# Kernel optimization log

Measured on AMD Instinct MI355X. Metric: run time of the kernel, lower is better.

Reference implementation:

```python
import jax, jax.numpy as jnp
import numpy as np

B, NVIS, NHID, NCLASS = 2048, 2048, 1024, 64


def setup_inputs() -> dict:
    key = jax.random.key(0)
    k1, k2, k3, k4, k5 = jax.random.split(key, 5)
    return {
        "v": jax.random.normal(k1, (B, NVIS), dtype=jnp.float32),
        "W": jax.random.normal(k2, (NVIS, NHID), dtype=jnp.float32),
        "c": jax.random.normal(k3, (1, NHID), dtype=jnp.float32),
        "d": jax.random.normal(k4, (1, NCLASS), dtype=jnp.float32),
        "U": jax.random.normal(k5, (NCLASS, NHID), dtype=jnp.float32),
    }


def reference(v, W, c, d, U):
    # precomputed_factor: [B, nhid]
    pre = jnp.matmul(v, W) + c
    # class free energies F[b, y] = d[0, y] + sum_j softplus(pre[b, j] + U[y, j])
    # broadcast to [B, nclass, nhid], reduce over hidden units
    F = d[0] + jnp.sum(jax.nn.softplus(pre[:, None, :] + U[None, :, :]), axis=-1)  # [B, nclass]
    # pairwise normalization 1 / sum_d exp(F_d - F_c) == softmax(F) along classes
    class_probs = jax.nn.softmax(F, axis=1)
    max_idx = jnp.argmax(class_probs, axis=1)
    one_hot = jax.nn.one_hot(max_idx, U.shape[0], dtype=jnp.int32)
    return class_probs, one_hot
```

## Files before the change

### kernel.cpp

```cpp
#include <hip/hip_runtime.h>

constexpr int kB    = 2048;
constexpr int kVIS  = 2048;
constexpr int kHID  = 1024;
constexpr int kCLS  = 64;
constexpr float kLog2e = 1.4426950408889634f;

typedef __attribute__((ext_vector_type(8))) short bf16x8;
typedef __attribute__((ext_vector_type(4))) float f32x4;
typedef __attribute__((ext_vector_type(2))) float f32x2;

typedef __attribute__((address_space(3))) unsigned       as3_u32;
typedef __attribute__((address_space(1))) const unsigned as1_u32;

__device__ __forceinline__ void g2lds16(const void* g, void* l) {
    __builtin_amdgcn_global_load_lds((as1_u32*)g, (as3_u32*)l, 16, 0, 0);
}

__device__ __forceinline__ unsigned short f2bf(float x) {
    unsigned u = __float_as_uint(x);
    u += 0x7fffu + ((u >> 16) & 1u);
    return (unsigned short)(u >> 16);
}
__device__ __forceinline__ float bf2f(unsigned short h) {
    return __uint_as_float(((unsigned)h) << 16);
}

__global__ __launch_bounds__(256) void prep_all(const float* __restrict__ v,
                                                const float* __restrict__ W,
                                                const float* __restrict__ U,
                                                unsigned short* __restrict__ vh,
                                                unsigned short* __restrict__ vl,
                                                unsigned short* __restrict__ wth,
                                                unsigned short* __restrict__ wtl,
                                                float* __restrict__ Utp) {
    __shared__ float T[64][65];
    const int bx = blockIdx.x;
    if (bx < 4096) {
        const int i = (bx * 256 + threadIdx.x) * 4;
        const float4 xv = *(const float4*)(v + i);
        ushort4 h, l;
        h.x = f2bf(xv.x); l.x = f2bf(xv.x - bf2f(h.x));
        h.y = f2bf(xv.y); l.y = f2bf(xv.y - bf2f(h.y));
        h.z = f2bf(xv.z); l.z = f2bf(xv.z - bf2f(h.z));
        h.w = f2bf(xv.w); l.w = f2bf(xv.w - bf2f(h.w));
        *(ushort4*)(vh + i) = h;
        *(ushort4*)(vl + i) = l;
    } else if (bx < 4608) {
        const int b = bx - 4096;
        const int n0 = (b & 15) * 64;
        const int k0 = (b >> 4) * 64;
        const int c = threadIdx.x & 63, r0 = threadIdx.x >> 6;
#pragma unroll
        for (int ps = 0; ps < 16; ++ps) {
            const int r = r0 + ps * 4;
            T[r][c] = W[(size_t)(k0 + r) * kHID + n0 + c];
        }
        __syncthreads();
#pragma unroll
        for (int ps = 0; ps < 16; ++ps) {
            const int nn = r0 + ps * 4;
            const float x = T[c][nn];
            const unsigned short h = f2bf(x);
            const unsigned short l = f2bf(x - bf2f(h));
            const size_t o = (size_t)(n0 + nn) * kVIS + k0 + c;
            wth[o] = h;
            wtl[o] = l;
        }
    } else {
        const int id = (bx - 4608) * 256 + threadIdx.x;
        const int j = id >> 6, y = id & 63;
        Utp[(((j >> 2) * kCLS + y) << 2) + (j & 3)] = U[(size_t)y * kHID + j] * kLog2e;
    }
}

__global__ __launch_bounds__(512, 4) void gemm_fused(const unsigned short* __restrict__ vh,
                                                     const unsigned short* __restrict__ vl,
                                                     const unsigned short* __restrict__ wth,
                                                     const unsigned short* __restrict__ wtl,
                                                     const float* __restrict__ cvec,
                                                     const float* __restrict__ Utp,
                                                     float* __restrict__ Fpart) {
    __shared__ __align__(16) union SMem {
        unsigned short stage[2][4][64 * 64];
        float psH[2][64][68];
    } smem;

    const int tid = threadIdx.x;
    const int lane = tid & 63, wave = tid >> 6;
    const int mh = wave >> 2;
    const int nh = (wave >> 1) & 1;
    const int kh = wave & 1;

    const int bid = blockIdx.x;
    const int idx = bid >> 3;
    const int mstripe = ((bid & 7) << 2) + (idx >> 4);
    const int ncol = idx & 15;
    const int m0 = mstripe * 64, n0 = ncol * 64;

    const int r = tid >> 3;
    const int oc = (((tid & 7) ^ ((tid >> 3) & 7)) << 3);
    const size_t ga = (size_t)(m0 + r) * kVIS + oc;
    const size_t gb = (size_t)(n0 + r) * kVIS + oc;
    const int ls = (r << 6) + ((tid & 7) << 3);

    const int fm = lane & 15, fq = lane >> 4;
    const int rx = fm & 7;
    const int ar0 = (mh * 32 + fm) << 6, ar1 = (mh * 32 + 16 + fm) << 6;
    const int br0 = (nh * 32 + fm) << 6, br1 = (nh * 32 + 16 + fm) << 6;
    const int p = (((kh << 2) + fq) ^ rx) << 3;

    f32x4 acc[2][2] = {};

    {
        g2lds16(vh + ga,  smem.stage[0][0] + ls);
        g2lds16(vl + ga,  smem.stage[0][1] + ls);
        g2lds16(wth + gb, smem.stage[0][2] + ls);
        g2lds16(wtl + gb, smem.stage[0][3] + ls);
    }
    __syncthreads();

    int cur = 0;
    for (int k0 = 0; k0 < kVIS; k0 += 64) {
        if (k0 + 64 < kVIS) {
            const int ko = k0 + 64;
            g2lds16(vh + ga + ko,  smem.stage[cur ^ 1][0] + ls);
            g2lds16(vl + ga + ko,  smem.stage[cur ^ 1][1] + ls);
            g2lds16(wth + gb + ko, smem.stage[cur ^ 1][2] + ls);
            g2lds16(wtl + gb + ko, smem.stage[cur ^ 1][3] + ls);
        }
        const unsigned short* Ah = smem.stage[cur][0];
        const unsigned short* Al = smem.stage[cur][1];
        const unsigned short* Bh = smem.stage[cur][2];
        const unsigned short* Bl = smem.stage[cur][3];
        const bf16x8 a_h0 = *(const bf16x8*)(Ah + ar0 + p);
        const bf16x8 a_h1 = *(const bf16x8*)(Ah + ar1 + p);
        const bf16x8 a_l0 = *(const bf16x8*)(Al + ar0 + p);
        const bf16x8 a_l1 = *(const bf16x8*)(Al + ar1 + p);
        const bf16x8 b_h0 = *(const bf16x8*)(Bh + br0 + p);
        const bf16x8 b_h1 = *(const bf16x8*)(Bh + br1 + p);
        const bf16x8 b_l0 = *(const bf16x8*)(Bl + br0 + p);
        const bf16x8 b_l1 = *(const bf16x8*)(Bl + br1 + p);
        acc[0][0] = __builtin_amdgcn_mfma_f32_16x16x32_bf16(a_h0, b_h0, acc[0][0], 0, 0, 0);
        acc[0][0] = __builtin_amdgcn_mfma_f32_16x16x32_bf16(a_h0, b_l0, acc[0][0], 0, 0, 0);
        acc[0][0] = __builtin_amdgcn_mfma_f32_16x16x32_bf16(a_l0, b_h0, acc[0][0], 0, 0, 0);
        acc[0][1] = __builtin_amdgcn_mfma_f32_16x16x32_bf16(a_h0, b_h1, acc[0][1], 0, 0, 0);
        acc[0][1] = __builtin_amdgcn_mfma_f32_16x16x32_bf16(a_h0, b_l1, acc[0][1], 0, 0, 0);
        acc[0][1] = __builtin_amdgcn_mfma_f32_16x16x32_bf16(a_l0, b_h1, acc[0][1], 0, 0, 0);
        acc[1][0] = __builtin_amdgcn_mfma_f32_16x16x32_bf16(a_h1, b_h0, acc[1][0], 0, 0, 0);
        acc[1][0] = __builtin_amdgcn_mfma_f32_16x16x32_bf16(a_h1, b_l0, acc[1][0], 0, 0, 0);
        acc[1][0] = __builtin_amdgcn_mfma_f32_16x16x32_bf16(a_l1, b_h0, acc[1][0], 0, 0, 0);
        acc[1][1] = __builtin_amdgcn_mfma_f32_16x16x32_bf16(a_h1, b_h1, acc[1][1], 0, 0, 0);
        acc[1][1] = __builtin_amdgcn_mfma_f32_16x16x32_bf16(a_h1, b_l1, acc[1][1], 0, 0, 0);
        acc[1][1] = __builtin_amdgcn_mfma_f32_16x16x32_bf16(a_l1, b_h1, acc[1][1], 0, 0, 0);
        __syncthreads();
        cur ^= 1;
    }

#pragma unroll
    for (int j = 0; j < 2; ++j) {
        const int col = nh * 32 + j * 16 + fm;
        const float cadd = kh ? 0.f : cvec[n0 + col];
#pragma unroll
        for (int i = 0; i < 2; ++i) {
            const int rbase = mh * 32 + i * 16 + fq * 4;
#pragma unroll
            for (int rr = 0; rr < 4; ++rr)
                smem.psH[kh][rbase + rr][col] = (acc[i][j][rr] + cadd) * kLog2e;
        }
    }
    __syncthreads();

#pragma unroll
    for (int s = 0; s < 2; ++s) {
        const int id = tid + (s << 9);
        const int row = id >> 4, q = id & 15;
        float4* d = (float4*)&smem.psH[0][row][q << 2];
        const float4* a = (const float4*)&smem.psH[1][row][q << 2];
        const float4 va = *a, vd = *d;
        *d = make_float4(vd.x + va.x, vd.y + va.y, vd.z + va.z, vd.w + va.w);
    }
    __syncthreads();

    const int q0 = (n0 >> 2);
    f32x2 relu2[8], prod2[8];
#pragma unroll
    for (int rr = 0; rr < 8; ++rr) { relu2[rr] = (f32x2)(0.f); prod2[rr] = (f32x2)(1.f); }

    const f32x2 zero2 = (f32x2)(0.f);
    for (int jc = 0; jc < 64; jc += 8) {
        const float4 ua = ((const float4*)Utp)[(q0 + (jc >> 2) + 0) * kCLS + lane];
        const float4 ub = ((const float4*)Utp)[(q0 + (jc >> 2) + 1) * kCLS + lane];
        const f32x2 u01 = {ua.x, ua.y}, u23 = {ua.z, ua.w};
        const f32x2 u45 = {ub.x, ub.y}, u67 = {ub.z, ub.w};
#pragma unroll
        for (int rr = 0; rr < 8; ++rr) {
            const int row = wave * 8 + rr;
            const float4 p0 = *(const float4*)&smem.psH[0][row][jc];
            const float4 p1 = *(const float4*)&smem.psH[0][row][jc + 4];
            f32x2 tp[4];
            tp[0] = (f32x2){p0.x, p0.y} + u01;
            tp[1] = (f32x2){p0.z, p0.w} + u23;
            tp[2] = (f32x2){p1.x, p1.y} + u45;
            tp[3] = (f32x2){p1.z, p1.w} + u67;
#pragma unroll
            for (int g = 0; g < 4; ++g) {
                const f32x2 t = tp[g];
                f32x2 e;
                e.x = __builtin_amdgcn_exp2f(-__builtin_fabsf(t.x));
                e.y = __builtin_amdgcn_exp2f(-__builtin_fabsf(t.y));
                prod2[rr] = __builtin_elementwise_fma(prod2[rr], e, prod2[rr]);
                relu2[rr] += __builtin_elementwise_max(t, zero2);
            }
        }
    }
#pragma unroll
    for (int rr = 0; rr < 8; ++rr) {
        const float contrib = relu2[rr].x + relu2[rr].y +
                              __builtin_amdgcn_logf(prod2[rr].x * prod2[rr].y);
        Fpart[((size_t)ncol * kB + m0 + wave * 8 + rr) * kCLS + lane] = contrib;
    }
}

__global__ __launch_bounds__(256) void softmax_final(const float* __restrict__ Fpart,
                                                     const float* __restrict__ dvec,
                                                     float* __restrict__ out) {
    const int tid = threadIdx.x;
    const int lane = tid & 63, wave = tid >> 6;
    const int row = blockIdx.x * 4 + wave;
    double s = 0.0;
#pragma unroll
    for (int k = 0; k < kHID / 64; ++k)
        s += (double)Fpart[((size_t)k * kB + row) * kCLS + lane];
    const float G = (float)s + dvec[lane] * kLog2e;

    float m = G;
    int mi = lane;
#pragma unroll
    for (int off = 32; off; off >>= 1) {
        const float om = __shfl_xor(m, off);
        const int   oi = __shfl_xor(mi, off);
        if (om > m || (om == m && oi < mi)) { m = om; mi = oi; }
    }
    const float e2 = __builtin_amdgcn_exp2f(G - m);
    float ssum = e2;
#pragma unroll
    for (int off = 32; off; off >>= 1) ssum += __shfl_xor(ssum, off);
    out[(size_t)row * kCLS + lane] = e2 / ssum;
    out[(size_t)kB * kCLS + (size_t)row * kCLS + lane] = (lane == mi) ? 1.0f : 0.0f;
}

constexpr int BM = 64, BN = 64, BK = 16;

__global__ __launch_bounds__(256) void gemm_vw(const float* __restrict__ V,
                                               const float* __restrict__ Wm,
                                               const float* __restrict__ cvec,
                                               float* __restrict__ pre) {
    __shared__ float As[BK][BM + 4];
    __shared__ float Bs[BK][BN + 4];
    const int tid = threadIdx.x;
    const int tx = tid & 15, ty = tid >> 4;
    const int m0 = blockIdx.y * BM, n0 = blockIdx.x * BN;
    const int arow = tid >> 2, acol = (tid & 3) << 2;
    const int brow = tid >> 4, bcol = (tid & 15) << 2;
    const float* vptr = V + (size_t)(m0 + arow) * kVIS + acol;
    const float* wptr = Wm + (size_t)brow * kHID + n0 + bcol;
    float acc[4][4] = {};
    for (int k0 = 0; k0 < kVIS; k0 += BK) {
        const float4 a4 = *(const float4*)(vptr + k0);
        const float4 b4 = *(const float4*)(wptr + (size_t)k0 * kHID);
        __syncthreads();
        As[acol + 0][arow] = a4.x; As[acol + 1][arow] = a4.y;
        As[acol + 2][arow] = a4.z; As[acol + 3][arow] = a4.w;
        *(float4*)&Bs[brow][bcol] = b4;
        __syncthreads();
#pragma unroll
        for (int k = 0; k < BK; ++k) {
            const float4 av = *(const float4*)&As[k][ty << 2];
            const float4 bv = *(const float4*)&Bs[k][tx << 2];
            const float a[4] = {av.x, av.y, av.z, av.w};
            const float b[4] = {bv.x, bv.y, bv.z, bv.w};
#pragma unroll
            for (int i = 0; i < 4; ++i)
#pragma unroll
                for (int j = 0; j < 4; ++j) acc[i][j] += a[i] * b[j];
        }
    }
#pragma unroll
    for (int i = 0; i < 4; ++i) {
        const int row = m0 + (ty << 2) + i;
        const int col = n0 + (tx << 2);
        const float4 cv = *(const float4*)(cvec + col);
        float4 o;
        o.x = acc[i][0] + cv.x; o.y = acc[i][1] + cv.y;
        o.z = acc[i][2] + cv.z; o.w = acc[i][3] + cv.w;
        *(float4*)(pre + (size_t)row * kHID + col) = o;
    }
}

__device__ __forceinline__ float softplus_f(float x) {
    return fmaxf(x, 0.f) + __logf(1.f + __expf(-fabsf(x)));
}

__global__ __launch_bounds__(256) void classify(const float* __restrict__ pre,
                                                const float* __restrict__ U,
                                                const float* __restrict__ dvec,
                                                float* __restrict__ out) {
    __shared__ float preS[4][kHID];
    __shared__ float Fs[4][kCLS];
    const int tid = threadIdx.x;
    const int lane = tid & 63, wave = tid >> 6;
    const int b0 = blockIdx.x * 4;
    const float4* src = (const float4*)(pre + (size_t)b0 * kHID);
    float4* dst = (float4*)preS;
    for (int i = tid; i < kHID; i += 256) dst[i] = src[i];
    __syncthreads();
    for (int yi = 0; yi < 16; ++yi) {
        const int y = (wave << 4) + yi;
        const float* Uy = U + (size_t)y * kHID;
        float a0 = 0.f, a1 = 0.f, a2 = 0.f, a3 = 0.f;
#pragma unroll
        for (int it = 0; it < kHID / 64; ++it) {
            const int j = lane + (it << 6);
            const float u = Uy[j];
            a0 += softplus_f(preS[0][j] + u);
            a1 += softplus_f(preS[1][j] + u);
            a2 += softplus_f(preS[2][j] + u);
            a3 += softplus_f(preS[3][j] + u);
        }
        double d0 = a0, d1 = a1, d2 = a2, d3 = a3;
#pragma unroll
        for (int off = 32; off; off >>= 1) {
            d0 += __shfl_xor(d0, off); d1 += __shfl_xor(d1, off);
            d2 += __shfl_xor(d2, off); d3 += __shfl_xor(d3, off);
        }
        if (lane == 0) {
            const float dy = dvec[y];
            Fs[0][y] = (float)d0 + dy; Fs[1][y] = (float)d1 + dy;
            Fs[2][y] = (float)d2 + dy; Fs[3][y] = (float)d3 + dy;
        }
    }
    __syncthreads();
    const float F = Fs[wave][lane];
    float m = F; int mi = lane;
#pragma unroll
    for (int off = 32; off; off >>= 1) {
        const float om = __shfl_xor(m, off);
        const int oi = __shfl_xor(mi, off);
        if (om > m || (om == m && oi < mi)) { m = om; mi = oi; }
    }
    const float e = __expf(F - m);
    float s = e;
#pragma unroll
    for (int off = 32; off; off >>= 1) s += __shfl_xor(s, off);
    const int row = b0 + wave;
    out[(size_t)row * kCLS + lane] = e / s;
    out[(size_t)kB * kCLS + (size_t)row * kCLS + lane] = (lane == mi) ? 1.0f : 0.0f;
}

extern "C" void kernel_launch(void* const* d_in, const int* in_sizes, int n_in,
                              void* d_out, int out_size, void* d_ws, size_t ws_size,
                              hipStream_t stream) {
    const float* v = (const float*)d_in[0];
    const float* W = (const float*)d_in[1];
    const float* c = (const float*)d_in[2];
    const float* d = (const float*)d_in[3];
    const float* U = (const float*)d_in[4];
    float* out = (float*)d_out;
    char* ws = (char*)d_ws;

    const size_t need = 33816576;
    if (ws_size >= need) {
        unsigned short* vh  = (unsigned short*)(ws);
        unsigned short* vl  = (unsigned short*)(ws + 8388608);
        unsigned short* wth = (unsigned short*)(ws + 16777216);
        unsigned short* wtl = (unsigned short*)(ws + 20971520);
        float* Utp   = (float*)(ws + 25165824);
        float* Fpart = (float*)(ws + 25427968);
        prep_all<<<4864, 256, 0, stream>>>(v, W, U, vh, vl, wth, wtl, Utp);
        gemm_fused<<<512, 512, 0, stream>>>(vh, vl, wth, wtl, c, Utp, Fpart);
        softmax_final<<<kB / 4, 256, 0, stream>>>(Fpart, d, out);
    } else {
        float* pre = (float*)ws;
        gemm_vw<<<dim3(kHID / BN, kB / BM), 256, 0, stream>>>(v, W, c, pre);
        classify<<<kB / 4, 256, 0, stream>>>(pre, U, d, out);
    }
}
```

Before: 130.0 us.

## Fuse prep, GEMM and softmax into one cooperative kernel with grid syncs

Merges the three kernel launches (bf16 split/transpose prep, fused GEMM+softplus, softmax/argmax) into a single cooperative kernel of 512 blocks. The stages are separated by grid-wide barriers, which removes launch gaps and inter-kernel drain. The old three-kernel path stays as a fallback if the cooperative launch fails. The cost is two grid syncs and all blocks having to be co-resident. The prep stage now runs with a fixed 512-block shape, and the softmax stage uses only half the waves of each block.

```diff
diff --git a/kernel.cpp b/kernel.cpp
--- a/kernel.cpp
+++ b/kernel.cpp
@@ -1,4 +1,7 @@
 #include <hip/hip_runtime.h>
+#include <hip/hip_cooperative_groups.h>
+
+namespace cg = cooperative_groups;
 
 constexpr int kB    = 2048;
 constexpr int kVIS  = 2048;
@@ -26,73 +29,76 @@
     return __uint_as_float(((unsigned)h) << 16);
 }
 
-__global__ __launch_bounds__(256) void prep_all(const float* __restrict__ v,
-                                                const float* __restrict__ W,
-                                                const float* __restrict__ U,
-                                                unsigned short* __restrict__ vh,
-                                                unsigned short* __restrict__ vl,
-                                                unsigned short* __restrict__ wth,
-                                                unsigned short* __restrict__ wtl,
-                                                float* __restrict__ Utp) {
-    __shared__ float T[64][65];
-    const int bx = blockIdx.x;
-    if (bx < 4096) {
-        const int i = (bx * 256 + threadIdx.x) * 4;
-        const float4 xv = *(const float4*)(v + i);
-        ushort4 h, l;
-        h.x = f2bf(xv.x); l.x = f2bf(xv.x - bf2f(h.x));
-        h.y = f2bf(xv.y); l.y = f2bf(xv.y - bf2f(h.y));
-        h.z = f2bf(xv.z); l.z = f2bf(xv.z - bf2f(h.z));
-        h.w = f2bf(xv.w); l.w = f2bf(xv.w - bf2f(h.w));
-        *(ushort4*)(vh + i) = h;
-        *(ushort4*)(vl + i) = l;
-    } else if (bx < 4608) {
-        const int b = bx - 4096;
-        const int n0 = (b & 15) * 64;
-        const int k0 = (b >> 4) * 64;
-        const int c = threadIdx.x & 63, r0 = threadIdx.x >> 6;
-#pragma unroll
-        for (int ps = 0; ps < 16; ++ps) {
-            const int r = r0 + ps * 4;
-            T[r][c] = W[(size_t)(k0 + r) * kHID + n0 + c];
+__global__ __launch_bounds__(512, 4) void fused_all(const float* __restrict__ v,
+                                                    const float* __restrict__ W,
+                                                    const float* __restrict__ U,
+                                                    const float* __restrict__ cvec,
+                                                    const float* __restrict__ dvec,
+                                                    unsigned short* __restrict__ vh,
+                                                    unsigned short* __restrict__ vl,
+                                                    unsigned short* __restrict__ wth,
+                                                    unsigned short* __restrict__ wtl,
+                                                    float* __restrict__ Utp,
+                                                    float* __restrict__ Fpart,
+                                                    float* __restrict__ out) {
+    __shared__ __align__(16) union SMem {
+        unsigned short stage[2][4][64 * 64];
+        float psH[2][64][68];
+        float T[64][65];
+    } smem;
+
+    const int tid = threadIdx.x;
+    const int bid = blockIdx.x;
+    const int lane = tid & 63, wave = tid >> 6;
+
+    {
+        const int gthr = bid * 512 + tid;
+#pragma unroll
+        for (int it = 0; it < 4; ++it) {
+            const int i = (gthr + it * 262144) * 4;
+            const float4 xv = *(const float4*)(v + i);
+            ushort4 h, l;
+            h.x = f2bf(xv.x); l.x = f2bf(xv.x - bf2f(h.x));
+            h.y = f2bf(xv.y); l.y = f2bf(xv.y - bf2f(h.y));
+            h.z = f2bf(xv.z); l.z = f2bf(xv.z - bf2f(h.z));
+            h.w = f2bf(xv.w); l.w = f2bf(xv.w - bf2f(h.w));
+            *(ushort4*)(vh + i) = h;
+            *(ushort4*)(vl + i) = l;
+        }
+    }
+    {
+        const int n0 = (bid & 15) * 64;
+        const int k0 = (bid >> 4) * 64;
+        const int c = lane, r0 = wave;
+#pragma unroll
+        for (int ps = 0; ps < 8; ++ps) {
+            const int r = r0 + ps * 8;
+            smem.T[r][c] = W[(size_t)(k0 + r) * kHID + n0 + c];
         }
         __syncthreads();
 #pragma unroll
-        for (int ps = 0; ps < 16; ++ps) {
-            const int nn = r0 + ps * 4;
-            const float x = T[c][nn];
+        for (int ps = 0; ps < 8; ++ps) {
+            const int nn = r0 + ps * 8;
+            const float x = smem.T[c][nn];
             const unsigned short h = f2bf(x);
             const unsigned short l = f2bf(x - bf2f(h));
             const size_t o = (size_t)(n0 + nn) * kVIS + k0 + c;
             wth[o] = h;
             wtl[o] = l;
         }
-    } else {
-        const int id = (bx - 4608) * 256 + threadIdx.x;
+    }
+    if (tid < 128) {
+        const int id = bid * 128 + tid;
         const int j = id >> 6, y = id & 63;
         Utp[(((j >> 2) * kCLS + y) << 2) + (j & 3)] = U[(size_t)y * kHID + j] * kLog2e;
     }
-}
-
-__global__ __launch_bounds__(512, 4) void gemm_fused(const unsigned short* __restrict__ vh,
-                                                     const unsigned short* __restrict__ vl,
-                                                     const unsigned short* __restrict__ wth,
-                                                     const unsigned short* __restrict__ wtl,
-                                                     const float* __restrict__ cvec,
-                                                     const float* __restrict__ Utp,
-                                                     float* __restrict__ Fpart) {
-    __shared__ __align__(16) union SMem {
-        unsigned short stage[2][4][64 * 64];
-        float psH[2][64][68];
-    } smem;
-
-    const int tid = threadIdx.x;
-    const int lane = tid & 63, wave = tid >> 6;
+
+    cg::this_grid().sync();
+
     const int mh = wave >> 2;
     const int nh = (wave >> 1) & 1;
     const int kh = wave & 1;
 
-    const int bid = blockIdx.x;
     const int idx = bid >> 3;
     const int mstripe = ((bid & 7) << 2) + (idx >> 4);
     const int ncol = idx & 15;
@@ -220,6 +226,228 @@
                               __builtin_amdgcn_logf(prod2[rr].x * prod2[rr].y);
         Fpart[((size_t)ncol * kB + m0 + wave * 8 + rr) * kCLS + lane] = contrib;
     }
+
+    cg::this_grid().sync();
+
+    if (wave < 4) {
+        const int row = bid * 4 + wave;
+        double s = 0.0;
+#pragma unroll
+        for (int k = 0; k < kHID / 64; ++k)
+            s += (double)Fpart[((size_t)k * kB + row) * kCLS + lane];
+        const float G = (float)s + dvec[lane] * kLog2e;
+
+        float m = G;
+        int mi = lane;
+#pragma unroll
+        for (int off = 32; off; off >>= 1) {
+            const float om = __shfl_xor(m, off);
+            const int   oi = __shfl_xor(mi, off);
+            if (om > m || (om == m && oi < mi)) { m = om; mi = oi; }
+        }
+        const float e2 = __builtin_amdgcn_exp2f(G - m);
+        float ssum = e2;
+#pragma unroll
+        for (int off = 32; off; off >>= 1) ssum += __shfl_xor(ssum, off);
+        out[(size_t)row * kCLS + lane] = e2 / ssum;
+        out[(size_t)kB * kCLS + (size_t)row * kCLS + lane] = (lane == mi) ? 1.0f : 0.0f;
+    }
+}
+
+__global__ __launch_bounds__(256) void prep_all(const float* __restrict__ v,
+                                                const float* __restrict__ W,
+                                                const float* __restrict__ U,
+                                                unsigned short* __restrict__ vh,
+                                                unsigned short* __restrict__ vl,
+                                                unsigned short* __restrict__ wth,
+                                                unsigned short* __restrict__ wtl,
+                                                float* __restrict__ Utp) {
+    __shared__ float T[64][65];
+    const int bx = blockIdx.x;
+    if (bx < 4096) {
+        const int i = (bx * 256 + threadIdx.x) * 4;
+        const float4 xv = *(const float4*)(v + i);
+        ushort4 h, l;
+        h.x = f2bf(xv.x); l.x = f2bf(xv.x - bf2f(h.x));
+        h.y = f2bf(xv.y); l.y = f2bf(xv.y - bf2f(h.y));
+        h.z = f2bf(xv.z); l.z = f2bf(xv.z - bf2f(h.z));
+        h.w = f2bf(xv.w); l.w = f2bf(xv.w - bf2f(h.w));
+        *(ushort4*)(vh + i) = h;
+        *(ushort4*)(vl + i) = l;
+    } else if (bx < 4608) {
+        const int b = bx - 4096;
+        const int n0 = (b & 15) * 64;
+        const int k0 = (b >> 4) * 64;
+        const int c = threadIdx.x & 63, r0 = threadIdx.x >> 6;
+#pragma unroll
+        for (int ps = 0; ps < 16; ++ps) {
+            const int r = r0 + ps * 4;
+            T[r][c] = W[(size_t)(k0 + r) * kHID + n0 + c];
+        }
+        __syncthreads();
+#pragma unroll
+        for (int ps = 0; ps < 16; ++ps) {
+            const int nn = r0 + ps * 4;
+            const float x = T[c][nn];
+            const unsigned short h = f2bf(x);
+            const unsigned short l = f2bf(x - bf2f(h));
+            const size_t o = (size_t)(n0 + nn) * kVIS + k0 + c;
+            wth[o] = h;
+            wtl[o] = l;
+        }
+    } else {
+        const int id = (bx - 4608) * 256 + threadIdx.x;
+        const int j = id >> 6, y = id & 63;
+        Utp[(((j >> 2) * kCLS + y) << 2) + (j & 3)] = U[(size_t)y * kHID + j] * kLog2e;
+    }
+}
+
+__global__ __launch_bounds__(512, 4) void gemm_fused(const unsigned short* __restrict__ vh,
+                                                     const unsigned short* __restrict__ vl,
+                                                     const unsigned short* __restrict__ wth,
+                                                     const unsigned short* __restrict__ wtl,
+                                                     const float* __restrict__ cvec,
+                                                     const float* __restrict__ Utp,
+                                                     float* __restrict__ Fpart) {
+    __shared__ __align__(16) union SMem {
+        unsigned short stage[2][4][64 * 64];
+        float psH[2][64][68];
+    } smem;
+
+    const int tid = threadIdx.x;
+    const int lane = tid & 63, wave = tid >> 6;
+    const int mh = wave >> 2;
+    const int nh = (wave >> 1) & 1;
+    const int kh = wave & 1;
+
+    const int bid = blockIdx.x;
+    const int idx = bid >> 3;
+    const int mstripe = ((bid & 7) << 2) + (idx >> 4);
+    const int ncol = idx & 15;
+    const int m0 = mstripe * 64, n0 = ncol * 64;
+
+    const int r = tid >> 3;
+    const int oc = (((tid & 7) ^ ((tid >> 3) & 7)) << 3);
+    const size_t ga = (size_t)(m0 + r) * kVIS + oc;
+    const size_t gb = (size_t)(n0 + r) * kVIS + oc;
+    const int ls = (r << 6) + ((tid & 7) << 3);
+
+    const int fm = lane & 15, fq = lane >> 4;
+    const int rx = fm & 7;
+    const int ar0 = (mh * 32 + fm) << 6, ar1 = (mh * 32 + 16 + fm) << 6;
+    const int br0 = (nh * 32 + fm) << 6, br1 = (nh * 32 + 16 + fm) << 6;
+    const int p = (((kh << 2) + fq) ^ rx) << 3;
+
+    f32x4 acc[2][2] = {};
+
+    {
+        g2lds16(vh + ga,  smem.stage[0][0] + ls);
+        g2lds16(vl + ga,  smem.stage[0][1] + ls);
+        g2lds16(wth + gb, smem.stage[0][2] + ls);
+        g2lds16(wtl + gb, smem.stage[0][3] + ls);
+    }
+    __syncthreads();
+
+    int cur = 0;
+    for (int k0 = 0; k0 < kVIS; k0 += 64) {
+        if (k0 + 64 < kVIS) {
+            const int ko = k0 + 64;
+            g2lds16(vh + ga + ko,  smem.stage[cur ^ 1][0] + ls);
+            g2lds16(vl + ga + ko,  smem.stage[cur ^ 1][1] + ls);
+            g2lds16(wth + gb + ko, smem.stage[cur ^ 1][2] + ls);
+            g2lds16(wtl + gb + ko, smem.stage[cur ^ 1][3] + ls);
+        }
+        const unsigned short* Ah = smem.stage[cur][0];
+        const unsigned short* Al = smem.stage[cur][1];
+        const unsigned short* Bh = smem.stage[cur][2];
+        const unsigned short* Bl = smem.stage[cur][3];
+        const bf16x8 a_h0 = *(const bf16x8*)(Ah + ar0 + p);
+        const bf16x8 a_h1 = *(const bf16x8*)(Ah + ar1 + p);
+        const bf16x8 a_l0 = *(const bf16x8*)(Al + ar0 + p);
+        const bf16x8 a_l1 = *(const bf16x8*)(Al + ar1 + p);
+        const bf16x8 b_h0 = *(const bf16x8*)(Bh + br0 + p);
+        const bf16x8 b_h1 = *(const bf16x8*)(Bh + br1 + p);
+        const bf16x8 b_l0 = *(const bf16x8*)(Bl + br0 + p);
+        const bf16x8 b_l1 = *(const bf16x8*)(Bl + br1 + p);
+        acc[0][0] = __builtin_amdgcn_mfma_f32_16x16x32_bf16(a_h0, b_h0, acc[0][0], 0, 0, 0);
+        acc[0][0] = __builtin_amdgcn_mfma_f32_16x16x32_bf16(a_h0, b_l0, acc[0][0], 0, 0, 0);
+        acc[0][0] = __builtin_amdgcn_mfma_f32_16x16x32_bf16(a_l0, b_h0, acc[0][0], 0, 0, 0);
+        acc[0][1] = __builtin_amdgcn_mfma_f32_16x16x32_bf16(a_h0, b_h1, acc[0][1], 0, 0, 0);
+        acc[0][1] = __builtin_amdgcn_mfma_f32_16x16x32_bf16(a_h0, b_l1, acc[0][1], 0, 0, 0);
+        acc[0][1] = __builtin_amdgcn_mfma_f32_16x16x32_bf16(a_l0, b_h1, acc[0][1], 0, 0, 0);
+        acc[1][0] = __builtin_amdgcn_mfma_f32_16x16x32_bf16(a_h1, b_h0, acc[1][0], 0, 0, 0);
+        acc[1][0] = __builtin_amdgcn_mfma_f32_16x16x32_bf16(a_h1, b_l0, acc[1][0], 0, 0, 0);
+        acc[1][0] = __builtin_amdgcn_mfma_f32_16x16x32_bf16(a_l1, b_h0, acc[1][0], 0, 0, 0);
+        acc[1][1] = __builtin_amdgcn_mfma_f32_16x16x32_bf16(a_h1, b_h1, acc[1][1], 0, 0, 0);
+        acc[1][1] = __builtin_amdgcn_mfma_f32_16x16x32_bf16(a_h1, b_l1, acc[1][1], 0, 0, 0);
+        acc[1][1] = __builtin_amdgcn_mfma_f32_16x16x32_bf16(a_l1, b_h1, acc[1][1], 0, 0, 0);
+        __syncthreads();
+        cur ^= 1;
+    }
+
+#pragma unroll
+    for (int j = 0; j < 2; ++j) {
+        const int col = nh * 32 + j * 16 + fm;
+        const float cadd = kh ? 0.f : cvec[n0 + col];
+#pragma unroll
+        for (int i = 0; i < 2; ++i) {
+            const int rbase = mh * 32 + i * 16 + fq * 4;
+#pragma unroll
+            for (int rr = 0; rr < 4; ++rr)
+                smem.psH[kh][rbase + rr][col] = (acc[i][j][rr] + cadd) * kLog2e;
+        }
+    }
+    __syncthreads();
+
+#pragma unroll
+    for (int s = 0; s < 2; ++s) {
+        const int id = tid + (s << 9);
+        const int row = id >> 4, q = id & 15;
+        float4* d = (float4*)&smem.psH[0][row][q << 2];
+        const float4* a = (const float4*)&smem.psH[1][row][q << 2];
+        const float4 va = *a, vd = *d;
+        *d = make_float4(vd.x + va.x, vd.y + va.y, vd.z + va.z, vd.w + va.w);
+    }
+    __syncthreads();
+
+    const int q0 = (n0 >> 2);
+    f32x2 relu2[8], prod2[8];
+#pragma unroll
+    for (int rr = 0; rr < 8; ++rr) { relu2[rr] = (f32x2)(0.f); prod2[rr] = (f32x2)(1.f); }
+
+    const f32x2 zero2 = (f32x2)(0.f);
+    for (int jc = 0; jc < 64; jc += 8) {
+        const float4 ua = ((const float4*)Utp)[(q0 + (jc >> 2) + 0) * kCLS + lane];
+        const float4 ub = ((const float4*)Utp)[(q0 + (jc >> 2) + 1) * kCLS + lane];
+        const f32x2 u01 = {ua.x, ua.y}, u23 = {ua.z, ua.w};
+        const f32x2 u45 = {ub.x, ub.y}, u67 = {ub.z, ub.w};
+#pragma unroll
+        for (int rr = 0; rr < 8; ++rr) {
+            const int row = wave * 8 + rr;
+            const float4 p0 = *(const float4*)&smem.psH[0][row][jc];
+            const float4 p1 = *(const float4*)&smem.psH[0][row][jc + 4];
+            f32x2 tp[4];
+            tp[0] = (f32x2){p0.x, p0.y} + u01;
+            tp[1] = (f32x2){p0.z, p0.w} + u23;
+            tp[2] = (f32x2){p1.x, p1.y} + u45;
+            tp[3] = (f32x2){p1.z, p1.w} + u67;
+#pragma unroll
+            for (int g = 0; g < 4; ++g) {
+                const f32x2 t = tp[g];
+                f32x2 e;
+                e.x = __builtin_amdgcn_exp2f(-__builtin_fabsf(t.x));
+                e.y = __builtin_amdgcn_exp2f(-__builtin_fabsf(t.y));
+                prod2[rr] = __builtin_elementwise_fma(prod2[rr], e, prod2[rr]);
+                relu2[rr] += __builtin_elementwise_max(t, zero2);
+            }
+        }
+    }
+#pragma unroll
+    for (int rr = 0; rr < 8; ++rr) {
+        const float contrib = relu2[rr].x + relu2[rr].y +
+                              __builtin_amdgcn_logf(prod2[rr].x * prod2[rr].y);
+        Fpart[((size_t)ncol * kB + m0 + wave * 8 + rr) * kCLS + lane] = contrib;
+    }
 }
 
 __global__ __launch_bounds__(256) void softmax_final(const float* __restrict__ Fpart,
@@ -377,9 +605,18 @@
         unsigned short* wtl = (unsigned short*)(ws + 20971520);
         float* Utp   = (float*)(ws + 25165824);
         float* Fpart = (float*)(ws + 25427968);
-        prep_all<<<4864, 256, 0, stream>>>(v, W, U, vh, vl, wth, wtl, Utp);
-        gemm_fused<<<512, 512, 0, stream>>>(vh, vl, wth, wtl, c, Utp, Fpart);
-        softmax_final<<<kB / 4, 256, 0, stream>>>(Fpart, d, out);
+
+        void* kargs[] = {(void*)&v, (void*)&W, (void*)&U, (void*)&c, (void*)&d,
+                         (void*)&vh, (void*)&vl, (void*)&wth, (void*)&wtl,
+                         (void*)&Utp, (void*)&Fpart, (void*)&out};
+        hipError_t err = hipLaunchCooperativeKernel((const void*)fused_all,
+                                                    dim3(512), dim3(512),
+                                                    kargs, 0, stream);
+        if (err != hipSuccess) {
+            prep_all<<<4864, 256, 0, stream>>>(v, W, U, vh, vl, wth, wtl, Utp);
+            gemm_fused<<<512, 512, 0, stream>>>(vh, vl, wth, wtl, c, Utp, Fpart);
+            softmax_final<<<kB / 4, 256, 0, stream>>>(Fpart, d, out);
+        }
     } else {
         float* pre = (float*)ws;
         gemm_vw<<<dim3(kHID / BN, kB / BM), 256, 0, stream>>>(v, W, c, pre);
```

Measured after the change: 252.2 us. 1.94x slower.

## Use four-stage LDS ring with k-step-32 tiles and parity-split waves

Applied to the files above, without the earlier changes.

The GEMM mainloop now streams K in 32-wide chunks that pack hi and lo bf16 halves into one 64-column tile. Chunks go into a 4-deep LDS ring and are prefetched two steps ahead, with explicit vmcnt waits and a raw s_barrier in place of a full __syncthreads per step. Instead of splitting each K tile across wave pairs, even and odd waves alternate consuming whole chunks. This keeps more loads in flight and cuts barrier cost, but only half the waves issue MFMAs on any given step.

```diff
diff --git a/kernel.cpp b/kernel.cpp
--- a/kernel.cpp
+++ b/kernel.cpp
@@ -82,7 +82,7 @@
                                                      const float* __restrict__ Utp,
                                                      float* __restrict__ Fpart) {
     __shared__ __align__(16) union SMem {
-        unsigned short stage[2][4][64 * 64];
+        unsigned short stage[4][8192];
         float psH[2][64][68];
     } smem;
 
@@ -90,7 +90,7 @@
     const int lane = tid & 63, wave = tid >> 6;
     const int mh = wave >> 2;
     const int nh = (wave >> 1) & 1;
-    const int kh = wave & 1;
+    const int pw = wave & 1;
 
     const int bid = blockIdx.x;
     const int idx = bid >> 3;
@@ -98,49 +98,78 @@
     const int ncol = idx & 15;
     const int m0 = mstripe * 64, n0 = ncol * 64;
 
-    const int r = tid >> 3;
-    const int oc = (((tid & 7) ^ ((tid >> 3) & 7)) << 3);
-    const size_t ga = (size_t)(m0 + r) * kVIS + oc;
-    const size_t gb = (size_t)(n0 + r) * kVIS + oc;
-    const int ls = (r << 6) + ((tid & 7) << 3);
+    unsigned short* const st = &smem.stage[0][0];
+
+    {
+    }
+    const int sr = tid >> 3;
+    const int sq = tid & 7;
+    const int su = sq ^ (sr & 7);
+    const int soct = su & 3;
+    const unsigned short* srcA =
+        ((su >> 2) ? vl : vh) + (size_t)(m0 + sr) * kVIS + (soct << 3);
+    const unsigned short* srcB =
+        ((su >> 2) ? wtl : wth) + (size_t)(n0 + sr) * kVIS + (soct << 3);
+    const int lsA = tid << 3;
+    const int lsB = 4096 + (tid << 3);
 
     const int fm = lane & 15, fq = lane >> 4;
-    const int rx = fm & 7;
-    const int ar0 = (mh * 32 + fm) << 6, ar1 = (mh * 32 + 16 + fm) << 6;
-    const int br0 = (nh * 32 + fm) << 6, br1 = (nh * 32 + 16 + fm) << 6;
-    const int p = (((kh << 2) + fq) ^ rx) << 3;
+    const int ph = ((fq ^ (fm & 7)) << 3);
+    const int pl = ph ^ 32;
+    const int ar0 = (mh * 32 + fm) << 6, ar1 = ar0 + 1024;
+    const int br0 = 4096 + ((nh * 32 + fm) << 6), br1 = br0 + 1024;
 
     f32x4 acc[2][2] = {};
 
+    g2lds16(srcA, st + lsA);
+    g2lds16(srcB, st + lsB);
+    g2lds16(srcA + 32, st + 8192 + lsA);
+    g2lds16(srcB + 32, st + 8192 + lsB);
+
+    for (int t = 0; t < 62; ++t) {
+        const int koff = (t + 2) << 5;
+        unsigned short* const dst = st + (((t + 2) & 3) << 13);
+        g2lds16(srcA + koff, dst + lsA);
+        g2lds16(srcB + koff, dst + lsB);
+        asm volatile("s_waitcnt vmcnt(4)" ::: "memory");
+        __builtin_amdgcn_s_barrier();
+        if (pw == (t & 1)) {
+            const unsigned short* buf = st + ((t & 3) << 13);
+            const bf16x8 a_h0 = *(const bf16x8*)(buf + ar0 + ph);
+            const bf16x8 a_l0 = *(const bf16x8*)(buf + ar0 + pl);
+            const bf16x8 a_h1 = *(const bf16x8*)(buf + ar1 + ph);
+            const bf16x8 a_l1 = *(const bf16x8*)(buf + ar1 + pl);
+            const bf16x8 b_h0 = *(const bf16x8*)(buf + br0 + ph);
+            const bf16x8 b_l0 = *(const bf16x8*)(buf + br0 + pl);
+            const bf16x8 b_h1 = *(const bf16x8*)(buf + br1 + ph);
+            const bf16x8 b_l1 = *(const bf16x8*)(buf + br1 + pl);
+            acc[0][0] = __builtin_amdgcn_mfma_f32_16x16x32_bf16(a_h0, b_h0, acc[0][0], 0, 0, 0);
+            acc[0][0] = __builtin_amdgcn_mfma_f32_16x16x32_bf16(a_h0, b_l0, acc[0][0], 0, 0, 0);
+            acc[0][0] = __builtin_amdgcn_mfma_f32_16x16x32_bf16(a_l0, b_h0, acc[0][0], 0, 0, 0);
+            acc[0][1] = __builtin_amdgcn_mfma_f32_16x16x32_bf16(a_h0, b_h1, acc[0][1], 0, 0, 0);
+            acc[0][1] = __builtin_amdgcn_mfma_f32_16x16x32_bf16(a_h0, b_l1, acc[0][1], 0, 0, 0);
+            acc[0][1] = __builtin_amdgcn_mfma_f32_16x16x32_bf16(a_l0, b_h1, acc[0][1], 0, 0, 0);
+            acc[1][0] = __builtin_amdgcn_mfma_f32_16x16x32_bf16(a_h1, b_h0, acc[1][0], 0, 0, 0);
+            acc[1][0] = __builtin_amdgcn_mfma_f32_16x16x32_bf16(a_h1, b_l0, acc[1][0], 0, 0, 0);
+            acc[1][0] = __builtin_amdgcn_mfma_f32_16x16x32_bf16(a_l1, b_h0, acc[1][0], 0, 0, 0);
+            acc[1][1] = __builtin_amdgcn_mfma_f32_16x16x32_bf16(a_h1, b_h1, acc[1][1], 0, 0, 0);
+            acc[1][1] = __builtin_amdgcn_mfma_f32_16x16x32_bf16(a_h1, b_l1, acc[1][1], 0, 0, 0);
+            acc[1][1] = __builtin_amdgcn_mfma_f32_16x16x32_bf16(a_l1, b_h1, acc[1][1], 0, 0, 0);
+        }
+    }
+    asm volatile("s_waitcnt vmcnt(0)" ::: "memory");
+    __builtin_amdgcn_s_barrier();
     {
-        g2lds16(vh + ga,  smem.stage[0][0] + ls);
-        g2lds16(vl + ga,  smem.stage[0][1] + ls);
-        g2lds16(wth + gb, smem.stage[0][2] + ls);
-        g2lds16(wtl + gb, smem.stage[0][3] + ls);
-    }
-    __syncthreads();
-
-    int cur = 0;
-    for (int k0 = 0; k0 < kVIS; k0 += 64) {
-        if (k0 + 64 < kVIS) {
-            const int ko = k0 + 64;
-            g2lds16(vh + ga + ko,  smem.stage[cur ^ 1][0] + ls);
-            g2lds16(vl + ga + ko,  smem.stage[cur ^ 1][1] + ls);
-            g2lds16(wth + gb + ko, smem.stage[cur ^ 1][2] + ls);
-            g2lds16(wtl + gb + ko, smem.stage[cur ^ 1][3] + ls);
-        }
-        const unsigned short* Ah = smem.stage[cur][0];
-        const unsigned short* Al = smem.stage[cur][1];
-        const unsigned short* Bh = smem.stage[cur][2];
-        const unsigned short* Bl = smem.stage[cur][3];
-        const bf16x8 a_h0 = *(const bf16x8*)(Ah + ar0 + p);
-        const bf16x8 a_h1 = *(const bf16x8*)(Ah + ar1 + p);
-        const bf16x8 a_l0 = *(const bf16x8*)(Al + ar0 + p);
-        const bf16x8 a_l1 = *(const bf16x8*)(Al + ar1 + p);
-        const bf16x8 b_h0 = *(const bf16x8*)(Bh + br0 + p);
-        const bf16x8 b_h1 = *(const bf16x8*)(Bh + br1 + p);
-        const bf16x8 b_l0 = *(const bf16x8*)(Bl + br0 + p);
-        const bf16x8 b_l1 = *(const bf16x8*)(Bl + br1 + p);
+        const int t = 62 + pw;
+        const unsigned short* buf = st + ((t & 3) << 13);
+        const bf16x8 a_h0 = *(const bf16x8*)(buf + ar0 + ph);
+        const bf16x8 a_l0 = *(const bf16x8*)(buf + ar0 + pl);
+        const bf16x8 a_h1 = *(const bf16x8*)(buf + ar1 + ph);
+        const bf16x8 a_l1 = *(const bf16x8*)(buf + ar1 + pl);
+        const bf16x8 b_h0 = *(const bf16x8*)(buf + br0 + ph);
+        const bf16x8 b_l0 = *(const bf16x8*)(buf + br0 + pl);
+        const bf16x8 b_h1 = *(const bf16x8*)(buf + br1 + ph);
+        const bf16x8 b_l1 = *(const bf16x8*)(buf + br1 + pl);
         acc[0][0] = __builtin_amdgcn_mfma_f32_16x16x32_bf16(a_h0, b_h0, acc[0][0], 0, 0, 0);
         acc[0][0] = __builtin_amdgcn_mfma_f32_16x16x32_bf16(a_h0, b_l0, acc[0][0], 0, 0, 0);
         acc[0][0] = __builtin_amdgcn_mfma_f32_16x16x32_bf16(a_l0, b_h0, acc[0][0], 0, 0, 0);
@@ -153,20 +182,19 @@
         acc[1][1] = __builtin_amdgcn_mfma_f32_16x16x32_bf16(a_h1, b_h1, acc[1][1], 0, 0, 0);
         acc[1][1] = __builtin_amdgcn_mfma_f32_16x16x32_bf16(a_h1, b_l1, acc[1][1], 0, 0, 0);
         acc[1][1] = __builtin_amdgcn_mfma_f32_16x16x32_bf16(a_l1, b_h1, acc[1][1], 0, 0, 0);
-        __syncthreads();
-        cur ^= 1;
-    }
+    }
+    __syncthreads();
 
 #pragma unroll
     for (int j = 0; j < 2; ++j) {
         const int col = nh * 32 + j * 16 + fm;
-        const float cadd = kh ? 0.f : cvec[n0 + col];
+        const float cadd = pw ? 0.f : cvec[n0 + col];
 #pragma unroll
         for (int i = 0; i < 2; ++i) {
             const int rbase = mh * 32 + i * 16 + fq * 4;
 #pragma unroll
             for (int rr = 0; rr < 4; ++rr)
-                smem.psH[kh][rbase + rr][col] = (acc[i][j][rr] + cadd) * kLog2e;
+                smem.psH[pw][rbase + rr][col] = (acc[i][j][rr] + cadd) * kLog2e;
         }
     }
     __syncthreads();
```

Result: slower. 136.0 us (+4.6%).

## Use 128-row tiles with 1024-thread blocks and triple-buffered LDS pipeline

Applied to the files above, without the earlier changes.

The fused GEMM moves to 1024-thread blocks covering 128 rows by 64 columns, so each W tile is shared across twice as many rows, and the grid halves to 256 blocks. The two-stage double buffer becomes a three-slab ring with explicit vmcnt waits and raw barriers. This keeps two slabs of loads in flight while one is computed. The goal is to hide global-to-LDS latency and reduce redundant B loads, at the cost of lower occupancy (one block per CU) and fewer blocks than CUs. The epilogue sections not shown must also handle the larger 128-row tile, so correctness there is uncertain.

```diff
diff --git a/kernel.cpp b/kernel.cpp
--- a/kernel.cpp
+++ b/kernel.cpp
@@ -74,16 +74,17 @@
     }
 }
 
-__global__ __launch_bounds__(512, 4) void gemm_fused(const unsigned short* __restrict__ vh,
-                                                     const unsigned short* __restrict__ vl,
-                                                     const unsigned short* __restrict__ wth,
-                                                     const unsigned short* __restrict__ wtl,
-                                                     const float* __restrict__ cvec,
-                                                     const float* __restrict__ Utp,
-                                                     float* __restrict__ Fpart) {
+__global__ __launch_bounds__(1024, 1) void gemm_fused(const unsigned short* __restrict__ vh,
+                                                      const unsigned short* __restrict__ vl,
+                                                      const unsigned short* __restrict__ wth,
+                                                      const unsigned short* __restrict__ wtl,
+                                                      const float* __restrict__ cvec,
+                                                      const float* __restrict__ Utp,
+                                                      float* __restrict__ Fpart) {
+    constexpr int kSlabElems = 24576;
     __shared__ __align__(16) union SMem {
-        unsigned short stage[2][4][64 * 64];
-        float psH[2][64][68];
+        unsigned short stage[3][kSlabElems];
+        float psH[2][128][68];
     } smem;
 
     const int tid = threadIdx.x;
@@ -93,54 +94,48 @@
     const int kh = wave & 1;
 
     const int bid = blockIdx.x;
-    const int idx = bid >> 3;
-    const int mstripe = ((bid & 7) << 2) + (idx >> 4);
-    const int ncol = idx & 15;
-    const int m0 = mstripe * 64, n0 = ncol * 64;
-
-    const int r = tid >> 3;
-    const int oc = (((tid & 7) ^ ((tid >> 3) & 7)) << 3);
-    const size_t ga = (size_t)(m0 + r) * kVIS + oc;
-    const size_t gb = (size_t)(n0 + r) * kVIS + oc;
-    const int ls = (r << 6) + ((tid & 7) << 3);
+    const int x = bid & 7, s = bid >> 3;
+    const int ncol = (x << 1) | (s & 1);
+    const int mstripe = s >> 1;
+    const int m0 = mstripe << 7, n0 = ncol << 6;
+
+    const int rA = tid >> 3, qA = tid & 7;
+    const int octA = (qA ^ (rA & 7)) << 3;
+    const unsigned short* const srcAh = vh + (size_t)(m0 + rA) * kVIS + octA;
+    const unsigned short* const srcAl = vl + (size_t)(m0 + rA) * kVIS + octA;
+    const int tb = tid & 511;
+    const int rB = tb >> 3, qB = tb & 7;
+    const int octB = (qB ^ (rB & 7)) << 3;
+    const unsigned short* const srcB =
+        ((tid < 512) ? wth : wtl) + (size_t)(n0 + rB) * kVIS + octB;
+    const int dOff = tid << 3;
+
+    unsigned short* const st = &smem.stage[0][0];
 
     const int fm = lane & 15, fq = lane >> 4;
-    const int rx = fm & 7;
-    const int ar0 = (mh * 32 + fm) << 6, ar1 = (mh * 32 + 16 + fm) << 6;
-    const int br0 = (nh * 32 + fm) << 6, br1 = (nh * 32 + 16 + fm) << 6;
-    const int p = (((kh << 2) + fq) ^ rx) << 3;
+    const int p = (((kh << 2) + fq) ^ (fm & 7)) << 3;
+    const int ar0 = ((mh * 32 + fm) << 6) + p;
+    const int ar1 = ar0 + (16 << 6);
+    const int br0 = 16384 + ((nh * 32 + fm) << 6) + p;
+    const int br1 = br0 + (16 << 6);
 
     f32x4 acc[2][2] = {};
 
-    {
-        g2lds16(vh + ga,  smem.stage[0][0] + ls);
-        g2lds16(vl + ga,  smem.stage[0][1] + ls);
-        g2lds16(wth + gb, smem.stage[0][2] + ls);
-        g2lds16(wtl + gb, smem.stage[0][3] + ls);
-    }
-    __syncthreads();
-
-    int cur = 0;
-    for (int k0 = 0; k0 < kVIS; k0 += 64) {
-        if (k0 + 64 < kVIS) {
-            const int ko = k0 + 64;
-            g2lds16(vh + ga + ko,  smem.stage[cur ^ 1][0] + ls);
-            g2lds16(vl + ga + ko,  smem.stage[cur ^ 1][1] + ls);
-            g2lds16(wth + gb + ko, smem.stage[cur ^ 1][2] + ls);
-            g2lds16(wtl + gb + ko, smem.stage[cur ^ 1][3] + ls);
-        }
-        const unsigned short* Ah = smem.stage[cur][0];
-        const unsigned short* Al = smem.stage[cur][1];
-        const unsigned short* Bh = smem.stage[cur][2];
-        const unsigned short* Bl = smem.stage[cur][3];
-        const bf16x8 a_h0 = *(const bf16x8*)(Ah + ar0 + p);
-        const bf16x8 a_h1 = *(const bf16x8*)(Ah + ar1 + p);
-        const bf16x8 a_l0 = *(const bf16x8*)(Al + ar0 + p);
-        const bf16x8 a_l1 = *(const bf16x8*)(Al + ar1 + p);
-        const bf16x8 b_h0 = *(const bf16x8*)(Bh + br0 + p);
-        const bf16x8 b_h1 = *(const bf16x8*)(Bh + br1 + p);
-        const bf16x8 b_l0 = *(const bf16x8*)(Bl + br0 + p);
-        const bf16x8 b_l1 = *(const bf16x8*)(Bl + br1 + p);
+    auto stage_slab = [&](int slab, unsigned short* buf) {
+        const int koff = slab << 6;
+        g2lds16(srcAh + koff, buf + dOff);
+        g2lds16(srcAl + koff, buf + 8192 + dOff);
+        g2lds16(srcB + koff, buf + 16384 + dOff);
+    };
+    auto compute = [&](const unsigned short* buf) {
+        const bf16x8 a_h0 = *(const bf16x8*)(buf + ar0);
+        const bf16x8 a_h1 = *(const bf16x8*)(buf + ar1);
+        const bf16x8 a_l0 = *(const bf16x8*)(buf + 8192 + ar0);
+        const bf16x8 a_l1 = *(const bf16x8*)(buf + 8192 + ar1);
+        const bf16x8 b_h0 = *(const bf16x8*)(buf + br0);
+        const bf16x8 b_h1 = *(const bf16x8*)(buf + br1);
+        const bf16x8 b_l0 = *(const bf16x8*)(buf + 4096 + br0);
+        const bf16x8 b_l1 = *(const bf16x8*)(buf + 4096 + br1);
         acc[0][0] = __builtin_amdgcn_mfma_f32_16x16x32_bf16(a_h0, b_h0, acc[0][0], 0, 0, 0);
         acc[0][0] = __builtin_amdgcn_mfma_f32_16x16x32_bf16(a_h0, b_l0, acc[0][0], 0, 0, 0);
         acc[0][0] = __builtin_amdgcn_mfma_f32_16x16x32_bf16(a_l0, b_h0, acc[0][0], 0, 0, 0);
@@ -153,9 +148,30 @@
         acc[1][1] = __builtin_amdgcn_mfma_f32_16x16x32_bf16(a_h1, b_h1, acc[1][1], 0, 0, 0);
         acc[1][1] = __builtin_amdgcn_mfma_f32_16x16x32_bf16(a_h1, b_l1, acc[1][1], 0, 0, 0);
         acc[1][1] = __builtin_amdgcn_mfma_f32_16x16x32_bf16(a_l1, b_h1, acc[1][1], 0, 0, 0);
-        __syncthreads();
-        cur ^= 1;
-    }
+    };
+
+    stage_slab(0, st);
+    stage_slab(1, st + kSlabElems);
+
+    unsigned short* bufPrev = st + 2 * kSlabElems;
+    unsigned short* bufCur  = st;
+    unsigned short* bufNext = st + kSlabElems;
+
+    for (int t = 0; t < 31; ++t) {
+        asm volatile("s_waitcnt vmcnt(3)" ::: "memory");
+        __builtin_amdgcn_s_barrier();
+        __builtin_amdgcn_sched_barrier(0);
+        compute(bufCur);
+        __builtin_amdgcn_s_barrier();
+        __builtin_amdgcn_sched_barrier(0);
+        if (t < 30) stage_slab(t + 2, bufPrev);
+        unsigned short* tmp = bufPrev; bufPrev = bufCur; bufCur = bufNext; bufNext = tmp;
+    }
+    asm volatile("s_waitcnt vmcnt(0)" ::: "memory");
+    __builtin_amdgcn_s_barrier();
+    __builtin_amdgcn_sched_barrier(0);
+    compute(bufCur);
+    __syncthreads();
 
 #pragma unroll
     for (int j = 0; j < 2; ++j) {
@@ -172,8 +188,8 @@
     __syncthreads();
 
 #pragma unroll
-    for (int s = 0; s < 2; ++s) {
-        const int id = tid + (s << 9);
+    for (int s2 = 0; s2 < 2; ++s2) {
+        const int id = tid + (s2 << 10);
         const int row = id >> 4, q = id & 15;
         float4* d = (float4*)&smem.psH[0][row][q << 2];
         const float4* a = (const float4*)&smem.psH[1][row][q << 2];
@@ -378,7 +394,7 @@
         float* Utp   = (float*)(ws + 25165824);
         float* Fpart = (float*)(ws + 25427968);
         prep_all<<<4864, 256, 0, stream>>>(v, W, U, vh, vl, wth, wtl, Utp);
-        gemm_fused<<<512, 512, 0, stream>>>(vh, vl, wth, wtl, c, Utp, Fpart);
+        gemm_fused<<<256, 1024, 0, stream>>>(vh, vl, wth, wtl, c, Utp, Fpart);
         softmax_final<<<kB / 4, 256, 0, stream>>>(Fpart, d, out);
     } else {
         float* pre = (float*)ws;
```

Measured after the change: 130.2 us. Within noise of the previous version (+0.1%).
